# Kernel optimization log

Measured on AMD Instinct MI355X. Metric: run time of the kernel, lower is better.

The kernel has to match this reference:

```python
import jax, jax.numpy as jnp
import numpy as np
import math

D_K = 128
M_BYTES = 65536  # default M = 1024*64
B_C = math.ceil(M_BYTES / (4 * D_K))  # = 128 key-block size
SCALE = 1.0 / math.sqrt(D_K)


def setup_inputs() -> dict:
    key = jax.random.key(0)
    kq, kk, kv = jax.random.split(key, 3)
    shape = (2, 16, 2048, 128)  # (b, heads, seq, d_k)
    return {
        "Q": jax.random.normal(kq, shape, jnp.float32),
        "K": jax.random.normal(kk, shape, jnp.float32),
        "V": jax.random.normal(kv, shape, jnp.float32),
    }


def reference(Q, K, V):
    b, h, s, d = Q.shape
    nblk = s // B_C
    # [nblk, b, h, B_C, d] key/value blocks, scanned in order (matches outer j loop)
    Kb = jnp.transpose(K.reshape(b, h, nblk, B_C, d), (2, 0, 1, 3, 4))
    Vb = jnp.transpose(V.reshape(b, h, nblk, B_C, d), (2, 0, 1, 3, 4))
    j0s = jnp.arange(nblk) * B_C
    q_pos = jnp.arange(s)[:, None]          # [s,1]
    k_off = jnp.arange(B_C)[None, :]        # [1,B_C]

    O0 = jnp.zeros_like(Q)
    l0 = jnp.zeros((b, h, s, 1), Q.dtype)
    m0 = jnp.full((b, h, s, 1), -jnp.inf, Q.dtype)

    def step(carry, xs):
        O, l, m = carry
        Kj, Vj, j0 = xs
        S_ij = jnp.einsum('bhqd,bhkd->bhqk', Q, Kj) * SCALE  # [b,h,s,B_C]
        mask = (j0 + k_off) > q_pos                           # [s,B_C] causal
        S_ij = jnp.where(mask[None, None], -jnp.inf, S_ij)
        m_ij = S_ij.max(axis=-1, keepdims=True)
        m_new = jnp.maximum(m, m_ij)
        P = jnp.exp(S_ij - m_new)
        e_i = jnp.exp(m - m_new)
        e_ij = jnp.exp(m_ij - m_new)  # NOTE: extra factor, faithful to source's bug
        l_new = e_i * l + P.sum(axis=-1, keepdims=True)
        O_new = (e_i * l * O + e_ij * jnp.einsum('bhqk,bhkd->bhqd', P, Vj)) / l_new
        return (O_new, l_new, m_new), None

    (O, _, _), _ = jax.lax.scan(step, (O0, l0, m0), (Kb, Vb, j0s))
    return O
```

## Files before the change

kernel.cpp:

```cpp
#include <hip/hip_runtime.h>
#include <math.h>


using f16   = _Float16;
using f16x8 = __attribute__((ext_vector_type(8))) _Float16;
using f32x4 = __attribute__((ext_vector_type(4))) float;

#define SEQ 2048
#define DK  128
#define FA_SCALE 0.08838834764831843f

__global__ __launch_bounds__(256) void prep_kv(const float* __restrict__ K,
                                               const float* __restrict__ V,
                                               f16* __restrict__ Kh,
                                               f16* __restrict__ Vtp) {
  __shared__ float Vsh[128][132];
  const int st = blockIdx.x, bh = blockIdx.y, tid = threadIdx.x;
  const size_t blk = ((size_t)bh * SEQ + st * 128) * DK;

  const float* Ksrc = K + blk;
  f16* Kdst = Kh + blk;
#pragma unroll
  for (int i = 0; i < 8; ++i) {
    int u = tid + i * 256;
    float4 a = *(const float4*)(Ksrc + u * 8);
    float4 b = *(const float4*)(Ksrc + u * 8 + 4);
    f16x8 h;
    h[0] = (f16)a.x; h[1] = (f16)a.y; h[2] = (f16)a.z; h[3] = (f16)a.w;
    h[4] = (f16)b.x; h[5] = (f16)b.y; h[6] = (f16)b.z; h[7] = (f16)b.w;
    *(f16x8*)(Kdst + u * 8) = h;
  }

  const float* Vsrc = V + blk;
#pragma unroll
  for (int i = 0; i < 16; ++i) {
    int f = tid + i * 256;
    int k = f >> 5, c = f & 31;
    *(float4*)&Vsh[k][c * 4] = *(const float4*)(Vsrc + k * DK + c * 4);
  }
  __syncthreads();

  const int l = tid & 63, wv = tid >> 6;
  const int r = l & 15, dr = l >> 4;
  f16* Vdst = Vtp + (size_t)bh * DK * SEQ + st * 128;
#pragma unroll
  for (int it = 0; it < 8; ++it) {
    int d = wv * 32 + it * 4 + dr;
    f16x8 h;
#pragma unroll
    for (int o = 0; o < 8; ++o) {
      int k = 32 * (r >> 2) + 16 * (o >> 2) + 4 * (r & 3) + (o & 3);
      h[o] = (f16)Vsh[k][d];
    }
    *(f16x8*)(Vdst + (size_t)d * SEQ + r * 8) = h;
  }
}

__device__ __forceinline__ void gl_lds16(const void* g, void* l) {
  __builtin_amdgcn_global_load_lds(
      (const __attribute__((address_space(1))) unsigned int*)g,
      (__attribute__((address_space(3))) unsigned int*)l, 16, 0, 0);
}

__device__ __forceinline__ void stage32k(const char* gbase, size_t gstride,
                                         char* lds, int w, int lg, int ll) {
#pragma unroll
  for (int i = 0; i < 4; ++i) {
    int t = w * 4 + i;
    int row = t * 4 + lg;
    int blog = (ll * 16) ^ ((row & 7) << 4);
    gl_lds16(gbase + (size_t)row * gstride + blog, lds + t * 1024);
  }
}

__global__ __launch_bounds__(512, 2) void fa_fwd_f16(
    const float* __restrict__ Q, const f16* __restrict__ Kh,
    const f16* __restrict__ Vtp, float* __restrict__ O) {
  const int n = blockIdx.x;
  const int m = n >> 3;
  const int bh = (n & 7) * 4 + (m & 3);
  const int qt = 15 - (m >> 2);

  const int tid  = threadIdx.x;
  const int lane = tid & 63;
  const int w  = tid >> 6;
  const int ll = lane & 15;
  const int lg = lane >> 4;
  const int swz = (ll & 7) << 4;

  __shared__ __align__(16) f16 Ks[2][128 * 128];
  __shared__ __align__(16) f16 Vs[2][128 * 128];

  const float* QB = Q + (size_t)bh * SEQ * DK;
  const char*  KB = (const char*)(Kh + (size_t)bh * SEQ * DK);
  const char*  VB = (const char*)(Vtp + (size_t)bh * DK * SEQ);
  float*       OB = O + (size_t)bh * SEQ * DK;

  const int qrow = qt * 128 + w * 16 + ll;

  f16x8 qf[4];
#pragma unroll
  for (int dc = 0; dc < 4; ++dc) {
    const float* p = QB + (size_t)qrow * DK + dc * 32 + lg * 8;
    float4 a = *(const float4*)p, b = *(const float4*)(p + 4);
    f16x8 h;
    h[0] = (f16)a.x; h[1] = (f16)a.y; h[2] = (f16)a.z; h[3] = (f16)a.w;
    h[4] = (f16)b.x; h[5] = (f16)b.y; h[6] = (f16)b.z; h[7] = (f16)b.w;
    qf[dc] = h;
  }

  f32x4 u[8];
#pragma unroll
  for (int nn = 0; nn < 8; ++nn) u[nn] = 0;
  float m_run = -INFINITY, lsum = 0.f;

  stage32k(KB, 256, (char*)&Ks[0][0], w, lg, ll);
  stage32k(VB, 4096, (char*)&Vs[0][0], w, lg, ll);
  __syncthreads();

  for (int kb = 0; kb <= qt; ++kb) {
    const int cur = kb & 1;
    if (kb < qt) {
      stage32k(KB + (size_t)(kb + 1) * 32768, 256, (char*)&Ks[cur ^ 1][0], w, lg, ll);
      stage32k(VB + (size_t)(kb + 1) * 256, 4096, (char*)&Vs[cur ^ 1][0], w, lg, ll);
    }

    f32x4 s[8];
#pragma unroll
    for (int k16 = 0; k16 < 8; ++k16) s[k16] = 0;
    const char* Kc = (const char*)&Ks[cur][0];
    __builtin_amdgcn_s_setprio(1);
#pragma unroll
    for (int dc = 0; dc < 4; ++dc) {
      const int boff = (dc * 64 + lg * 16) ^ swz;
#pragma unroll
      for (int k16 = 0; k16 < 8; ++k16) {
        f16x8 kf = *(const f16x8*)(Kc + (k16 * 16 + ll) * 256 + boff);
        s[k16] = __builtin_amdgcn_mfma_f32_16x16x32_f16(kf, qf[dc], s[k16], 0, 0, 0);
      }
    }
    __builtin_amdgcn_s_setprio(0);

    float mx = -INFINITY;
    if (kb == qt) {
      const int kbase = kb * 128;
#pragma unroll
      for (int k16 = 0; k16 < 8; ++k16)
#pragma unroll
        for (int r = 0; r < 4; ++r) {
          float v = s[k16][r] * FA_SCALE;
          if (kbase + k16 * 16 + lg * 4 + r > qrow) v = -INFINITY;
          s[k16][r] = v;
          mx = fmaxf(mx, v);
        }
    } else {
#pragma unroll
      for (int k16 = 0; k16 < 8; ++k16)
#pragma unroll
        for (int r = 0; r < 4; ++r) {
          float v = s[k16][r] * FA_SCALE;
          s[k16][r] = v;
          mx = fmaxf(mx, v);
        }
    }
    mx = fmaxf(mx, __shfl_xor(mx, 16));
    mx = fmaxf(mx, __shfl_xor(mx, 32));

    const float mn = fmaxf(m_run, mx);
    const float ei = __expf(m_run - mn);
    const float ej = __expf(mx - mn);
    m_run = mn;

    float ps = 0.f;
#pragma unroll
    for (int k16 = 0; k16 < 8; ++k16)
#pragma unroll
      for (int r = 0; r < 4; ++r) {
        float p = __expf(s[k16][r] - mn);
        s[k16][r] = p;
        ps += p;
      }
    ps += __shfl_xor(ps, 16);
    ps += __shfl_xor(ps, 32);
    lsum = ei * lsum + ps;

    f16x8 pa[4];
#pragma unroll
    for (int c = 0; c < 4; ++c) {
      f16x8 h;
#pragma unroll
      for (int r = 0; r < 4; ++r) {
        h[r]     = (f16)(s[2 * c][r] * ej);
        h[r + 4] = (f16)(s[2 * c + 1][r] * ej);
      }
      pa[c] = h;
    }

    const float eu0 = __shfl(ei, lg * 4 + 0);
    const float eu1 = __shfl(ei, lg * 4 + 1);
    const float eu2 = __shfl(ei, lg * 4 + 2);
    const float eu3 = __shfl(ei, lg * 4 + 3);
#pragma unroll
    for (int nn = 0; nn < 8; ++nn) {
      u[nn][0] *= eu0; u[nn][1] *= eu1; u[nn][2] *= eu2; u[nn][3] *= eu3;
    }

    const char* Vc = (const char*)&Vs[cur][0];
    __builtin_amdgcn_s_setprio(1);
#pragma unroll
    for (int c = 0; c < 4; ++c) {
      const int boff = (c * 64 + lg * 16) ^ swz;
#pragma unroll
      for (int nn = 0; nn < 8; ++nn) {
        f16x8 vf = *(const f16x8*)(Vc + (nn * 16 + ll) * 256 + boff);
        u[nn] = __builtin_amdgcn_mfma_f32_16x16x32_f16(pa[c], vf, u[nn], 0, 0, 0);
      }
    }
    __builtin_amdgcn_s_setprio(0);

    __syncthreads();
  }

  const float rl0 = 1.f / __shfl(lsum, lg * 4 + 0);
  const float rl1 = 1.f / __shfl(lsum, lg * 4 + 1);
  const float rl2 = 1.f / __shfl(lsum, lg * 4 + 2);
  const float rl3 = 1.f / __shfl(lsum, lg * 4 + 3);
  const size_t rbase = (size_t)(qt * 128 + w * 16 + lg * 4);
#pragma unroll
  for (int nn = 0; nn < 8; ++nn) {
    const int col = nn * 16 + ll;
    OB[(rbase + 0) * DK + col] = u[nn][0] * rl0;
    OB[(rbase + 1) * DK + col] = u[nn][1] * rl1;
    OB[(rbase + 2) * DK + col] = u[nn][2] * rl2;
    OB[(rbase + 3) * DK + col] = u[nn][3] * rl3;
  }
}

extern "C" void kernel_launch(void* const* d_in, const int* in_sizes, int n_in,
                              void* d_out, int out_size, void* d_ws, size_t ws_size,
                              hipStream_t stream) {
  const float* Q = (const float*)d_in[0];
  const float* K = (const float*)d_in[1];
  const float* V = (const float*)d_in[2];
  float* O = (float*)d_out;
  (void)in_sizes; (void)n_in; (void)out_size; (void)ws_size;

  f16* Kh  = (f16*)d_ws;
  f16* Vtp = (f16*)((char*)d_ws + 16777216);

  prep_kv<<<dim3(16, 32), 256, 0, stream>>>(K, V, Kh, Vtp);
  fa_fwd_f16<<<512, 512, 0, stream>>>(Q, Kh, Vtp, O);
}
```

Before: 192.3 us.

## Switch attention to 32x32x16 MFMA with 4 waves and single-buffered LDS

Rewrites the attention kernel to use 32x32x16 f16 MFMAs with 256-thread blocks, each wave owning 32 query rows, so fewer MFMA issues and LDS fragment loads are needed per tile. The P fragments are built in registers with permlane32 swaps, and row factors are broadcast through a small shared array. The scale is folded into Q at load time and V is no longer permuted in prep. The K/V LDS double buffer is dropped in favour of a single buffer loaded after each iteration. That removes copy/compute overlap and adds a second barrier per iteration, but halves LDS use.

```diff
diff --git a/kernel.cpp b/kernel.cpp
--- a/kernel.cpp
+++ b/kernel.cpp
@@ -2,9 +2,10 @@
 #include <math.h>
 
 
-using f16   = _Float16;
-using f16x8 = __attribute__((ext_vector_type(8))) _Float16;
-using f32x4 = __attribute__((ext_vector_type(4))) float;
+using f16    = _Float16;
+using f16x8  = __attribute__((ext_vector_type(8))) _Float16;
+using f32x16 = __attribute__((ext_vector_type(16))) float;
+typedef unsigned int uint32;
 
 #define SEQ 2048
 #define DK  128
@@ -13,7 +14,7 @@
 __global__ __launch_bounds__(256) void prep_kv(const float* __restrict__ K,
                                                const float* __restrict__ V,
                                                f16* __restrict__ Kh,
-                                               f16* __restrict__ Vtp) {
+                                               f16* __restrict__ Vt) {
   __shared__ float Vsh[128][132];
   const int st = blockIdx.x, bh = blockIdx.y, tid = threadIdx.x;
   const size_t blk = ((size_t)bh * SEQ + st * 128) * DK;
@@ -42,16 +43,13 @@
 
   const int l = tid & 63, wv = tid >> 6;
   const int r = l & 15, dr = l >> 4;
-  f16* Vdst = Vtp + (size_t)bh * DK * SEQ + st * 128;
+  f16* Vdst = Vt + (size_t)bh * DK * SEQ + st * 128;
 #pragma unroll
   for (int it = 0; it < 8; ++it) {
     int d = wv * 32 + it * 4 + dr;
     f16x8 h;
 #pragma unroll
-    for (int o = 0; o < 8; ++o) {
-      int k = 32 * (r >> 2) + 16 * (o >> 2) + 4 * (r & 3) + (o & 3);
-      h[o] = (f16)Vsh[k][d];
-    }
+    for (int o = 0; o < 8; ++o) h[o] = (f16)Vsh[r * 8 + o][d];
     *(f16x8*)(Vdst + (size_t)d * SEQ + r * 8) = h;
   }
 }
@@ -62,20 +60,26 @@
       (__attribute__((address_space(3))) unsigned int*)l, 16, 0, 0);
 }
 
-__device__ __forceinline__ void stage32k(const char* gbase, size_t gstride,
-                                         char* lds, int w, int lg, int ll) {
-#pragma unroll
-  for (int i = 0; i < 4; ++i) {
-    int t = w * 4 + i;
+__device__ __forceinline__ void stage_tile(const char* gbase, size_t gstride,
+                                           char* lds, int w, int lg, int ll) {
+#pragma unroll
+  for (int i = 0; i < 8; ++i) {
+    int t = w * 8 + i;
     int row = t * 4 + lg;
     int blog = (ll * 16) ^ ((row & 7) << 4);
     gl_lds16(gbase + (size_t)row * gstride + blog, lds + t * 1024);
   }
 }
 
-__global__ __launch_bounds__(512, 2) void fa_fwd_f16(
+__device__ __forceinline__ uint32 pkh(float x, float y) {
+  union { f16 h[2]; uint32 u; } t;
+  t.h[0] = (f16)x; t.h[1] = (f16)y;
+  return t.u;
+}
+
+__global__ __launch_bounds__(256, 2) void fa_fwd_f16(
     const float* __restrict__ Q, const f16* __restrict__ Kh,
-    const f16* __restrict__ Vtp, float* __restrict__ O) {
+    const f16* __restrict__ Vt, float* __restrict__ O) {
   const int n = blockIdx.x;
   const int m = n >> 3;
   const int bh = (n & 7) * 4 + (m & 3);
@@ -84,86 +88,80 @@
   const int tid  = threadIdx.x;
   const int lane = tid & 63;
   const int w  = tid >> 6;
+  const int li = lane & 31;
+  const int hi = lane >> 5;
+  const int lg = lane >> 4;
   const int ll = lane & 15;
-  const int lg = lane >> 4;
-  const int swz = (ll & 7) << 4;
-
-  __shared__ __align__(16) f16 Ks[2][128 * 128];
-  __shared__ __align__(16) f16 Vs[2][128 * 128];
+  const int rsw = (li & 7) << 4;
+
+  __shared__ __align__(16) f16 Ks[128 * 128];
+  __shared__ __align__(16) f16 Vs[128 * 128];
+  __shared__ float bc[4][32];
 
   const float* QB = Q + (size_t)bh * SEQ * DK;
   const char*  KB = (const char*)(Kh + (size_t)bh * SEQ * DK);
-  const char*  VB = (const char*)(Vtp + (size_t)bh * DK * SEQ);
+  const char*  VB = (const char*)(Vt + (size_t)bh * DK * SEQ);
   float*       OB = O + (size_t)bh * SEQ * DK;
 
-  const int qrow = qt * 128 + w * 16 + ll;
-
-  f16x8 qf[4];
-#pragma unroll
-  for (int dc = 0; dc < 4; ++dc) {
-    const float* p = QB + (size_t)qrow * DK + dc * 32 + lg * 8;
+  const int qrow = qt * 128 + w * 32 + li;
+
+  f16x8 qf[8];
+#pragma unroll
+  for (int ds = 0; ds < 8; ++ds) {
+    const float* p = QB + (size_t)qrow * DK + ds * 16 + hi * 8;
     float4 a = *(const float4*)p, b = *(const float4*)(p + 4);
     f16x8 h;
-    h[0] = (f16)a.x; h[1] = (f16)a.y; h[2] = (f16)a.z; h[3] = (f16)a.w;
-    h[4] = (f16)b.x; h[5] = (f16)b.y; h[6] = (f16)b.z; h[7] = (f16)b.w;
-    qf[dc] = h;
-  }
-
-  f32x4 u[8];
-#pragma unroll
-  for (int nn = 0; nn < 8; ++nn) u[nn] = 0;
+    h[0] = (f16)(a.x * FA_SCALE); h[1] = (f16)(a.y * FA_SCALE);
+    h[2] = (f16)(a.z * FA_SCALE); h[3] = (f16)(a.w * FA_SCALE);
+    h[4] = (f16)(b.x * FA_SCALE); h[5] = (f16)(b.y * FA_SCALE);
+    h[6] = (f16)(b.z * FA_SCALE); h[7] = (f16)(b.w * FA_SCALE);
+    qf[ds] = h;
+  }
+
+  f32x16 u[4];
+#pragma unroll
+  for (int dt = 0; dt < 4; ++dt) u[dt] = 0;
   float m_run = -INFINITY, lsum = 0.f;
 
-  stage32k(KB, 256, (char*)&Ks[0][0], w, lg, ll);
-  stage32k(VB, 4096, (char*)&Vs[0][0], w, lg, ll);
+  stage_tile(KB, 256, (char*)Ks, w, lg, ll);
+  stage_tile(VB, 4096, (char*)Vs, w, lg, ll);
   __syncthreads();
 
   for (int kb = 0; kb <= qt; ++kb) {
-    const int cur = kb & 1;
-    if (kb < qt) {
-      stage32k(KB + (size_t)(kb + 1) * 32768, 256, (char*)&Ks[cur ^ 1][0], w, lg, ll);
-      stage32k(VB + (size_t)(kb + 1) * 256, 4096, (char*)&Vs[cur ^ 1][0], w, lg, ll);
-    }
-
-    f32x4 s[8];
-#pragma unroll
-    for (int k16 = 0; k16 < 8; ++k16) s[k16] = 0;
-    const char* Kc = (const char*)&Ks[cur][0];
+    f32x16 s[4];
+#pragma unroll
+    for (int kt = 0; kt < 4; ++kt) s[kt] = 0;
     __builtin_amdgcn_s_setprio(1);
 #pragma unroll
-    for (int dc = 0; dc < 4; ++dc) {
-      const int boff = (dc * 64 + lg * 16) ^ swz;
-#pragma unroll
-      for (int k16 = 0; k16 < 8; ++k16) {
-        f16x8 kf = *(const f16x8*)(Kc + (k16 * 16 + ll) * 256 + boff);
-        s[k16] = __builtin_amdgcn_mfma_f32_16x16x32_f16(kf, qf[dc], s[k16], 0, 0, 0);
+    for (int ds = 0; ds < 8; ++ds) {
+      const int boff = (ds * 32 + hi * 16) ^ rsw;
+#pragma unroll
+      for (int kt = 0; kt < 4; ++kt) {
+        f16x8 kf = *(const f16x8*)((const char*)Ks + (kt * 32 + li) * 256 + boff);
+        s[kt] = __builtin_amdgcn_mfma_f32_32x32x16_f16(kf, qf[ds], s[kt], 0, 0, 0);
       }
     }
     __builtin_amdgcn_s_setprio(0);
 
     float mx = -INFINITY;
     if (kb == qt) {
-      const int kbase = kb * 128;
-#pragma unroll
-      for (int k16 = 0; k16 < 8; ++k16)
-#pragma unroll
-        for (int r = 0; r < 4; ++r) {
-          float v = s[k16][r] * FA_SCALE;
-          if (kbase + k16 * 16 + lg * 4 + r > qrow) v = -INFINITY;
-          s[k16][r] = v;
+      const int kb0 = kb * 128;
+#pragma unroll
+      for (int kt = 0; kt < 4; ++kt)
+#pragma unroll
+        for (int r = 0; r < 16; ++r) {
+          const int kg = kb0 + kt * 32 + (r & 3) + 8 * (r >> 2) + 4 * hi;
+          float v = s[kt][r];
+          if (kg > qrow) v = -INFINITY;
+          s[kt][r] = v;
           mx = fmaxf(mx, v);
         }
     } else {
 #pragma unroll
-      for (int k16 = 0; k16 < 8; ++k16)
-#pragma unroll
-        for (int r = 0; r < 4; ++r) {
-          float v = s[k16][r] * FA_SCALE;
-          s[k16][r] = v;
-          mx = fmaxf(mx, v);
-        }
-    }
-    mx = fmaxf(mx, __shfl_xor(mx, 16));
+      for (int kt = 0; kt < 4; ++kt)
+#pragma unroll
+        for (int r = 0; r < 16; ++r) mx = fmaxf(mx, s[kt][r]);
+    }
     mx = fmaxf(mx, __shfl_xor(mx, 32));
 
     const float mn = fmaxf(m_run, mx);
@@ -173,66 +171,66 @@
 
     float ps = 0.f;
 #pragma unroll
-    for (int k16 = 0; k16 < 8; ++k16)
-#pragma unroll
-      for (int r = 0; r < 4; ++r) {
-        float p = __expf(s[k16][r] - mn);
-        s[k16][r] = p;
+    for (int kt = 0; kt < 4; ++kt)
+#pragma unroll
+      for (int r = 0; r < 16; ++r) {
+        float p = __expf(s[kt][r] - mn);
+        s[kt][r] = p;
         ps += p;
       }
-    ps += __shfl_xor(ps, 16);
     ps += __shfl_xor(ps, 32);
     lsum = ei * lsum + ps;
 
-    f16x8 pa[4];
-#pragma unroll
-    for (int c = 0; c < 4; ++c) {
-      f16x8 h;
-#pragma unroll
-      for (int r = 0; r < 4; ++r) {
-        h[r]     = (f16)(s[2 * c][r] * ej);
-        h[r + 4] = (f16)(s[2 * c + 1][r] * ej);
+    bc[w][li] = ei;
+    float eu[16];
+#pragma unroll
+    for (int r = 0; r < 16; ++r)
+      eu[r] = bc[w][(r & 3) + 8 * (r >> 2) + 4 * hi];
+#pragma unroll
+    for (int dt = 0; dt < 4; ++dt)
+#pragma unroll
+      for (int r = 0; r < 16; ++r) u[dt][r] *= eu[r];
+
+    __builtin_amdgcn_s_setprio(1);
+#pragma unroll
+    for (int ks = 0; ks < 8; ++ks) {
+      const int kt = ks >> 1, b0 = (ks & 1) * 8;
+      uint32 A = pkh(s[kt][b0 + 0] * ej, s[kt][b0 + 1] * ej);
+      uint32 B = pkh(s[kt][b0 + 2] * ej, s[kt][b0 + 3] * ej);
+      uint32 C = pkh(s[kt][b0 + 4] * ej, s[kt][b0 + 5] * ej);
+      uint32 D = pkh(s[kt][b0 + 6] * ej, s[kt][b0 + 7] * ej);
+      asm("v_permlane32_swap_b32 %0, %1" : "+v"(A), "+v"(C));
+      asm("v_permlane32_swap_b32 %0, %1" : "+v"(B), "+v"(D));
+      union { uint32 w4[4]; f16x8 v; } pa;
+      pa.w4[0] = A; pa.w4[1] = B; pa.w4[2] = C; pa.w4[3] = D;
+      const int boff = (ks * 32 + hi * 16) ^ rsw;
+#pragma unroll
+      for (int dt = 0; dt < 4; ++dt) {
+        f16x8 vf = *(const f16x8*)((const char*)Vs + (dt * 32 + li) * 256 + boff);
+        u[dt] = __builtin_amdgcn_mfma_f32_32x32x16_f16(pa.v, vf, u[dt], 0, 0, 0);
       }
-      pa[c] = h;
-    }
-
-    const float eu0 = __shfl(ei, lg * 4 + 0);
-    const float eu1 = __shfl(ei, lg * 4 + 1);
-    const float eu2 = __shfl(ei, lg * 4 + 2);
-    const float eu3 = __shfl(ei, lg * 4 + 3);
-#pragma unroll
-    for (int nn = 0; nn < 8; ++nn) {
-      u[nn][0] *= eu0; u[nn][1] *= eu1; u[nn][2] *= eu2; u[nn][3] *= eu3;
-    }
-
-    const char* Vc = (const char*)&Vs[cur][0];
-    __builtin_amdgcn_s_setprio(1);
-#pragma unroll
-    for (int c = 0; c < 4; ++c) {
-      const int boff = (c * 64 + lg * 16) ^ swz;
-#pragma unroll
-      for (int nn = 0; nn < 8; ++nn) {
-        f16x8 vf = *(const f16x8*)(Vc + (nn * 16 + ll) * 256 + boff);
-        u[nn] = __builtin_amdgcn_mfma_f32_16x16x32_f16(pa[c], vf, u[nn], 0, 0, 0);
-      }
     }
     __builtin_amdgcn_s_setprio(0);
 
     __syncthreads();
-  }
-
-  const float rl0 = 1.f / __shfl(lsum, lg * 4 + 0);
-  const float rl1 = 1.f / __shfl(lsum, lg * 4 + 1);
-  const float rl2 = 1.f / __shfl(lsum, lg * 4 + 2);
-  const float rl3 = 1.f / __shfl(lsum, lg * 4 + 3);
-  const size_t rbase = (size_t)(qt * 128 + w * 16 + lg * 4);
-#pragma unroll
-  for (int nn = 0; nn < 8; ++nn) {
-    const int col = nn * 16 + ll;
-    OB[(rbase + 0) * DK + col] = u[nn][0] * rl0;
-    OB[(rbase + 1) * DK + col] = u[nn][1] * rl1;
-    OB[(rbase + 2) * DK + col] = u[nn][2] * rl2;
-    OB[(rbase + 3) * DK + col] = u[nn][3] * rl3;
+    if (kb < qt) {
+      stage_tile(KB + (size_t)(kb + 1) * 32768, 256, (char*)Ks, w, lg, ll);
+      stage_tile(VB + (size_t)(kb + 1) * 256, 4096, (char*)Vs, w, lg, ll);
+    }
+    __syncthreads();
+  }
+
+  bc[w][li] = lsum;
+  float rl[16];
+#pragma unroll
+  for (int r = 0; r < 16; ++r)
+    rl[r] = 1.0f / bc[w][(r & 3) + 8 * (r >> 2) + 4 * hi];
+#pragma unroll
+  for (int r = 0; r < 16; ++r) {
+    float* rowp =
+        OB + (size_t)(qt * 128 + w * 32 + (r & 3) + 8 * (r >> 2) + 4 * hi) * DK + li;
+#pragma unroll
+    for (int dt = 0; dt < 4; ++dt) rowp[dt * 32] = u[dt][r] * rl[r];
   }
 }
 
@@ -245,9 +243,9 @@
   float* O = (float*)d_out;
   (void)in_sizes; (void)n_in; (void)out_size; (void)ws_size;
 
-  f16* Kh  = (f16*)d_ws;
-  f16* Vtp = (f16*)((char*)d_ws + 16777216);
-
-  prep_kv<<<dim3(16, 32), 256, 0, stream>>>(K, V, Kh, Vtp);
-  fa_fwd_f16<<<512, 512, 0, stream>>>(Q, Kh, Vtp, O);
-}
+  f16* Kh = (f16*)d_ws;
+  f16* Vt = (f16*)((char*)d_ws + 16777216);
+
+  prep_kv<<<dim3(16, 32), 256, 0, stream>>>(K, V, Kh, Vt);
+  fa_fwd_f16<<<512, 256, 0, stream>>>(Q, Kh, Vt, O);
+}
```

After: 194.5 us. No clear change (+1.2%).
